# Kernel optimization log

Hardware: AMD Instinct MI355X
Metric: run time of the kernel (lower is better)

## Reference

```python
import jax, jax.numpy as jnp
import numpy as np

B, T, D = 8, 4096, 256
INNER, S = D * 2, 16          # expand=2, d_state=16
CODEBOOK, THRESH = 240, 0.7


def setup_inputs() -> dict:
    key = jax.random.key(0)
    ks = iter(jax.random.split(key, 32))
    nrm = lambda shape, s=0.02: jax.random.normal(next(ks), shape, dtype=jnp.float32) * s
    return {
        'x': jax.random.normal(next(ks), (B, T, D), dtype=jnp.float32),
        # Mamba backend params
        'in_proj_w': nrm((D, 2 * INNER)), 'in_proj_b': jnp.zeros((2 * INNER,), jnp.float32),
        'conv_proj_w': nrm((INNER, INNER)), 'conv_proj_b': jnp.zeros((INNER,), jnp.float32),
        'A_log': jax.random.normal(next(ks), (INNER, S), dtype=jnp.float32) * 0.01,
        'bc_proj_w': nrm((INNER, 2 * S)), 'bc_proj_b': jnp.zeros((2 * S,), jnp.float32),
        'dt_proj_w': nrm((INNER, INNER)), 'dt_proj_b': jnp.zeros((INNER,), jnp.float32),
        'out_proj_w': nrm((INNER, D)), 'out_proj_b': jnp.zeros((D,), jnp.float32),
        # CatastropheDetector params
        'cat1_w': nrm((D, 64)), 'cat1_b': jnp.zeros((64,), jnp.float32),
        'cat2_w': nrm((64, 32)), 'cat2_b': jnp.zeros((32,), jnp.float32),
        'risk_w': nrm((32, 1)), 'risk_b': jnp.zeros((1,), jnp.float32),
        # E8 quantizer params
        'e8a_w': nrm((D, 64)), 'e8a_b': jnp.zeros((64,), jnp.float32),
        'e8b_w': nrm((64, 8)), 'e8b_b': jnp.zeros((8,), jnp.float32),
        'e8_codebook': jax.random.normal(next(ks), (CODEBOOK, 8), dtype=jnp.float32) * 0.1,
    }


def reference(x, in_proj_w, in_proj_b, conv_proj_w, conv_proj_b, A_log,
              bc_proj_w, bc_proj_b, dt_proj_w, dt_proj_b, out_proj_w, out_proj_b,
              cat1_w, cat1_b, cat2_w, cat2_b, risk_w, risk_b,
              e8a_w, e8a_b, e8b_w, e8b_b, e8_codebook):
    # ---- Mamba selective-scan dynamics ----
    xp = x @ in_proj_w + in_proj_b                       # [B,T,2*inner]
    x_main, x_gate = jnp.split(xp, 2, axis=-1)
    x_conv = jax.nn.silu(x_main @ conv_proj_w + conv_proj_b)  # [B,T,inner]
    A = -jnp.exp(A_log)                                  # [inner,S]
    bc = x_conv @ bc_proj_w + bc_proj_b                  # [B,T,2S]
    Bp, Cp = jnp.split(bc, 2, axis=-1)                   # [B,T,S] each
    dt = jax.nn.softplus(x_conv @ dt_proj_w + dt_proj_b) # [B,T,inner]

    def step(h, ins):  # h: [B,inner,S]
        x_t, dt_t, B_t, C_t = ins                        # [B,inner],[B,inner],[B,S],[B,S]
        A_bar = jnp.exp(dt_t[..., None] * A)
        h = A_bar * h + (dt_t[..., None] * B_t[:, None, :]) * x_t[..., None]
        y_t = (h * C_t[:, None, :]).sum(-1)              # [B,inner]
        return h, y_t

    h0 = jnp.zeros((x.shape[0], A_log.shape[0], A_log.shape[1]), x.dtype)
    xs = (x_conv.transpose(1, 0, 2), dt.transpose(1, 0, 2),
          Bp.transpose(1, 0, 2), Cp.transpose(1, 0, 2))
    _, y = jax.lax.scan(step, h0, xs)                    # [T,B,inner]
    y = y.transpose(1, 0, 2) * jax.nn.silu(x_gate)
    y = y @ out_proj_w + out_proj_b                      # [B,T,D]

    # ---- Catastrophe / bifurcation detector ----
    f = jax.nn.gelu(y @ cat1_w + cat1_b)
    f = f @ cat2_w + cat2_b
    risk = jax.nn.sigmoid((f @ risk_w + risk_b).squeeze(-1))  # [B,T]
    vel = jnp.diff(y, axis=1, prepend=y[:, :1])
    vn = jnp.linalg.norm(vel, axis=-1)                   # [B,T]
    acc = jnp.abs(jnp.diff(vn, axis=1, prepend=vn[:, :1]))
    combined = 0.5 * risk + 0.3 * jax.nn.sigmoid(vn) + 0.2 * jax.nn.sigmoid(acc)
    is_bif = combined > THRESH

    # ---- E8 quantization with straight-through estimator ----
    e8c = jax.nn.gelu(y @ e8a_w + e8a_b) @ e8b_w + e8b_b # [B,T,8]
    flat = e8c.reshape(-1, 8)
    d2 = ((flat ** 2).sum(1, keepdims=True)
          - 2.0 * flat @ e8_codebook.T
          + (e8_codebook ** 2).sum(1)[None, :])          # [B*T,240]
    idx = jnp.argmin(d2, axis=1)
    q = e8_codebook[idx].reshape(e8c.shape)
    e8_codes = e8c + jax.lax.stop_gradient(q - e8c)
    return (y, e8_codes, idx.reshape(y.shape[0], y.shape[1]), is_bif)
```

## Files before the change

kernel.cpp:

```cpp
#include <hip/hip_runtime.h>
#include <hip/hip_bf16.h>
#include <math.h>

#define BB 8
#define TT 4096
#define DD 256
#define INNER 512
#define SS 16
#define MTOK (BB*TT)
#define NCODE 240

#define SCAN_NC 64
#define SCAN_L  64

typedef unsigned short u16;
typedef unsigned int   u32;
typedef __attribute__((ext_vector_type(8))) short short8;
typedef __attribute__((ext_vector_type(4))) float f32x4;

__device__ __forceinline__ float sigmoidf_(float x) { return 1.f / (1.f + expf(-x)); }
__device__ __forceinline__ float siluf_(float x)    { return x / (1.f + expf(-x)); }
__device__ __forceinline__ float geluf_(float x) {
    float x3 = x * x * x;
    return 0.5f * x * (1.f + tanhf(0.7978845608028654f * (x + 0.044715f * x3)));
}
__device__ __forceinline__ float softplusf_(float x) {
    return fmaxf(x, 0.f) + log1pf(expf(-fabsf(x)));
}

__device__ __forceinline__ u16 f2bf(float v) {
    u32 u = __float_as_uint(v);
    u32 r = (u + 0x7FFFu + ((u >> 16) & 1u)) >> 16;
    return (u16)r;
}
__device__ __forceinline__ float bf2f(u16 h) {
    return __uint_as_float(((u32)h) << 16);
}

__device__ __forceinline__ void gload16(const void* g, void* l) {
    __builtin_amdgcn_global_load_lds((const __attribute__((address_space(1))) u32*)g,
                                     (__attribute__((address_space(3))) u32*)l, 16, 0, 0);
}

template<int MODE>
__global__ __launch_bounds__(256)
void gemmS(const u16* __restrict__ Ah, const u16* __restrict__ Al, int K,
           const u16* __restrict__ BTh, const u16* __restrict__ BTl,
           const float* __restrict__ bias, int Nstore,
           float* __restrict__ out0, u16* __restrict__ oh, u16* __restrict__ ol)
{
    __shared__ u16 sm[4][128 * 32];

    const int tid  = threadIdx.x;
    const int lane = tid & 63;
    const int wv   = tid >> 6;
    const int wr   = wv >> 1;
    const int wc   = wv & 1;
    const int lc   = lane & 15;
    const int kc   = lane >> 4;
    const int row0 = blockIdx.y * 128;
    const int col0 = blockIdx.x * 128;

    const u16* Agh = Ah + (size_t)row0 * K;
    const u16* Agl = Al + (size_t)row0 * K;
    const u16* Bgh = BTh + (size_t)col0 * K;
    const u16* Bgl = BTl + (size_t)col0 * K;

    f32x4 acc[4][4];
    #pragma unroll
    for (int m = 0; m < 4; ++m)
        #pragma unroll
        for (int n = 0; n < 4; ++n) acc[m][n] = (f32x4)0.f;

    for (int k0 = 0; k0 < K; k0 += 32) {
        #pragma unroll
        for (int c = 0; c < 2; ++c) {
            int e = c * 256 + tid;
            int row = e >> 2, ch = e & 3;
            int chs = ch ^ ((row >> 1) & 3);
            size_t go = (size_t)row * K + k0 + chs * 8;
            gload16(Agh + go, &sm[0][e * 8]);
            gload16(Agl + go, &sm[1][e * 8]);
            gload16(Bgh + go, &sm[2][e * 8]);
            gload16(Bgl + go, &sm[3][e * 8]);
        }
        __syncthreads();

        short8 ah[4], al[4], bh[4], bl[4];
        #pragma unroll
        for (int m = 0; m < 4; ++m) {
            int row = wr * 64 + m * 16 + lc;
            int off = row * 32 + ((kc ^ ((row >> 1) & 3)) << 3);
            ah[m] = *(const short8*)&sm[0][off];
            al[m] = *(const short8*)&sm[1][off];
        }
        #pragma unroll
        for (int n = 0; n < 4; ++n) {
            int row = wc * 64 + n * 16 + lc;
            int off = row * 32 + ((kc ^ ((row >> 1) & 3)) << 3);
            bh[n] = *(const short8*)&sm[2][off];
            bl[n] = *(const short8*)&sm[3][off];
        }
        #pragma unroll
        for (int m = 0; m < 4; ++m)
            #pragma unroll
            for (int n = 0; n < 4; ++n) {
                acc[m][n] = __builtin_amdgcn_mfma_f32_16x16x32_bf16(ah[m], bh[n], acc[m][n], 0, 0, 0);
                acc[m][n] = __builtin_amdgcn_mfma_f32_16x16x32_bf16(ah[m], bl[n], acc[m][n], 0, 0, 0);
                acc[m][n] = __builtin_amdgcn_mfma_f32_16x16x32_bf16(al[m], bh[n], acc[m][n], 0, 0, 0);
            }
        __syncthreads();
    }

    #pragma unroll
    for (int n = 0; n < 4; ++n) {
        int colg = col0 + wc * 64 + n * 16 + lc;
        float bv = (MODE == 3) ? ((colg < Nstore) ? bias[colg] : 0.f) : bias[colg];
        #pragma unroll
        for (int m = 0; m < 4; ++m) {
            f32x4 a = acc[m][n];
            #pragma unroll
            for (int r = 0; r < 4; ++r) {
                int rowg = row0 + wr * 64 + m * 16 + kc * 4 + r;
                float v = a[r] + bv;
                if (MODE == 0) {
                    if (colg < 512) {
                        u16 hh = f2bf(v);
                        oh[(size_t)rowg * 512 + colg] = hh;
                        ol[(size_t)rowg * 512 + colg] = f2bf(v - bf2f(hh));
                    } else {
                        out0[(size_t)rowg * 512 + colg - 512] = v;
                    }
                } else if (MODE == 1) {
                    v = siluf_(v);
                    u16 hh = f2bf(v);
                    oh[(size_t)rowg * 512 + colg] = hh;
                    ol[(size_t)rowg * 512 + colg] = f2bf(v - bf2f(hh));
                } else if (MODE == 2) {
                    out0[(size_t)rowg * 512 + colg] = softplusf_(v);
                } else if (MODE == 3) {
                    if (colg < Nstore) out0[(size_t)rowg * 32 + colg] = v;
                } else if (MODE == 4) {
                    out0[(size_t)rowg * 256 + colg] = v;
                    u16 hh = f2bf(v);
                    oh[(size_t)rowg * 256 + colg] = hh;
                    ol[(size_t)rowg * 256 + colg] = f2bf(v - bf2f(hh));
                } else {
                    out0[(size_t)rowg * 128 + colg] = geluf_(v);
                }
            }
        }
    }
}

__global__ __launch_bounds__(256)
void split_kernel(const float* __restrict__ s, u16* __restrict__ h,
                  u16* __restrict__ l, int n)
{
    int i = blockIdx.x * 256 + threadIdx.x;
    if (i >= n) return;
    float v = s[i];
    u16 hh = f2bf(v);
    h[i] = hh;
    l[i] = f2bf(v - bf2f(hh));
}

__global__ __launch_bounds__(256)
void splitT_kernel(const float* __restrict__ w, u16* __restrict__ hT,
                   u16* __restrict__ lT, int K, int N, int Npad)
{
    int idx = blockIdx.x * 256 + threadIdx.x;
    if (idx >= Npad * K) return;
    int n = idx / K, k = idx - n * K;
    float v = (n < N) ? w[(size_t)k * N + n] : 0.f;
    u16 hh = f2bf(v);
    hT[idx] = hh;
    lT[idx] = f2bf(v - bf2f(hh));
}

__global__ __launch_bounds__(256)
void headprep_kernel(const float* __restrict__ c1w, const float* __restrict__ c1b,
                     const float* __restrict__ e8aw, const float* __restrict__ e8ab,
                     u16* __restrict__ hT, u16* __restrict__ lT, float* __restrict__ hb)
{
    int idx = blockIdx.x * 256 + threadIdx.x;
    if (idx < 128) hb[idx] = (idx < 64) ? c1b[idx] : e8ab[idx - 64];
    if (idx >= 128 * 256) return;
    int n = idx >> 8, k = idx & 255;
    float v = (n < 64) ? c1w[(size_t)k * 64 + n] : e8aw[(size_t)k * 64 + (n - 64)];
    u16 hh = f2bf(v);
    hT[idx] = hh;
    lT[idx] = f2bf(v - bf2f(hh));
}

__global__ __launch_bounds__(256)
void scan_pass1(const float* __restrict__ DT, const u16* __restrict__ XCh,
                const u16* __restrict__ XCl, const float* __restrict__ BC,
                const float* __restrict__ A_log,
                float* __restrict__ Pbuf, float* __restrict__ Hbuf)
{
    const int bid  = blockIdx.x;
    const int half = bid & 1;
    const int c    = (bid >> 1) & (SCAN_NC - 1);
    const int b    = bid >> 7;
    const int ch   = half * 256 + threadIdx.x;
    const int row0 = b * TT + c * SCAN_L;

    float A[16];
    {
        const float4* ar = (const float4*)(A_log + ch * 16);
        #pragma unroll
        for (int q = 0; q < 4; ++q) {
            float4 v = ar[q];
            A[q * 4 + 0] = -__expf(v.x);
            A[q * 4 + 1] = -__expf(v.y);
            A[q * 4 + 2] = -__expf(v.z);
            A[q * 4 + 3] = -__expf(v.w);
        }
    }

    float h[16];
    #pragma unroll
    for (int s = 0; s < 16; ++s) h[s] = 0.f;
    float dtsum = 0.f;

    const float* dtp = DT  + (size_t)row0 * 512 + ch;
    const u16*   xhp = XCh + (size_t)row0 * 512 + ch;
    const u16*   xlp = XCl + (size_t)row0 * 512 + ch;
    const float* bcp = BC  + (size_t)row0 * 32;

    float dv = dtp[0];
    float xv = bf2f(xhp[0]) + bf2f(xlp[0]);
    for (int t = 0; t < SCAN_L; ++t) {
        const int tn = (t + 1 < SCAN_L) ? t + 1 : t;
        float dvn = dtp[(size_t)tn * 512];
        float xvn = bf2f(xhp[(size_t)tn * 512]) + bf2f(xlp[(size_t)tn * 512]);
        const float* br = bcp + (size_t)t * 32;
        float dtx = dv * xv;
        dtsum += dv;
        #pragma unroll
        for (int s = 0; s < 16; ++s) {
            float a = __expf(dv * A[s]);
            h[s] = fmaf(a, h[s], dtx * br[s]);
        }
        dv = dvn; xv = xvn;
    }

    size_t o = ((size_t)(b * SCAN_NC + c) * 512 + ch) * 16;
    #pragma unroll
    for (int s = 0; s < 16; ++s) {
        Pbuf[o + s] = __expf(dtsum * A[s]);
        Hbuf[o + s] = h[s];
    }
}

__global__ __launch_bounds__(256)
void scan_pass2(const float* __restrict__ Pbuf, float* __restrict__ Hbuf)
{
    const int idx = blockIdx.x * 256 + threadIdx.x;
    const int b = idx >> 13;
    const int ds = idx & 8191;
    float hin = 0.f;
    for (int c = 0; c < SCAN_NC; ++c) {
        size_t o = ((size_t)(b * SCAN_NC + c)) * (INNER * SS) + ds;
        float p = Pbuf[o], hh = Hbuf[o];
        Hbuf[o] = hin;
        hin = fmaf(p, hin, hh);
    }
}

__global__ __launch_bounds__(256)
void scan_pass3(const float* __restrict__ DT, const u16* __restrict__ XCh,
                const u16* __restrict__ XCl, const float* __restrict__ BC,
                const float* __restrict__ A_log, const float* __restrict__ GATE,
                const float* __restrict__ Hin,
                u16* __restrict__ YGh, u16* __restrict__ YGl)
{
    const int bid  = blockIdx.x;
    const int half = bid & 1;
    const int c    = (bid >> 1) & (SCAN_NC - 1);
    const int b    = bid >> 7;
    const int ch   = half * 256 + threadIdx.x;
    const int row0 = b * TT + c * SCAN_L;

    float A[16];
    {
        const float4* ar = (const float4*)(A_log + ch * 16);
        #pragma unroll
        for (int q = 0; q < 4; ++q) {
            float4 v = ar[q];
            A[q * 4 + 0] = -__expf(v.x);
            A[q * 4 + 1] = -__expf(v.y);
            A[q * 4 + 2] = -__expf(v.z);
            A[q * 4 + 3] = -__expf(v.w);
        }
    }

    float h[16];
    {
        size_t o = ((size_t)(b * SCAN_NC + c) * 512 + ch) * 16;
        const float4* hr = (const float4*)(Hin + o);
        #pragma unroll
        for (int q = 0; q < 4; ++q) {
            float4 v = hr[q];
            h[q * 4 + 0] = v.x; h[q * 4 + 1] = v.y;
            h[q * 4 + 2] = v.z; h[q * 4 + 3] = v.w;
        }
    }

    const float* dtp = DT   + (size_t)row0 * 512 + ch;
    const u16*   xhp = XCh  + (size_t)row0 * 512 + ch;
    const u16*   xlp = XCl  + (size_t)row0 * 512 + ch;
    const float* gtp = GATE + (size_t)row0 * 512 + ch;
    const float* bcp = BC   + (size_t)row0 * 32;
    u16* yhp = YGh + (size_t)row0 * 512 + ch;
    u16* ylp = YGl + (size_t)row0 * 512 + ch;

    float dv = dtp[0];
    float xv = bf2f(xhp[0]) + bf2f(xlp[0]);
    float gv = gtp[0];
    for (int t = 0; t < SCAN_L; ++t) {
        const int tn = (t + 1 < SCAN_L) ? t + 1 : t;
        float dvn = dtp[(size_t)tn * 512];
        float xvn = bf2f(xhp[(size_t)tn * 512]) + bf2f(xlp[(size_t)tn * 512]);
        float gvn = gtp[(size_t)tn * 512];
        const float* br = bcp + (size_t)t * 32;
        float dtx = dv * xv;
        float y = 0.f;
        #pragma unroll
        for (int s = 0; s < 16; ++s) {
            float a = __expf(dv * A[s]);
            h[s] = fmaf(a, h[s], dtx * br[s]);
            y = fmaf(h[s], br[16 + s], y);
        }
        float yg = y * siluf_(gv);
        u16 hh = f2bf(yg);
        yhp[(size_t)t * 512] = hh;
        ylp[(size_t)t * 512] = f2bf(yg - bf2f(hh));
        dv = dvn; xv = xvn; gv = gvn;
    }
}

__global__ __launch_bounds__(256)
void head_finish(const float* __restrict__ F1,
                 const float* __restrict__ w2, const float* __restrict__ b2,
                 const float* __restrict__ w3, const float* __restrict__ b3,
                 const float* __restrict__ wb, const float* __restrict__ bb,
                 const float* __restrict__ cb,
                 float* __restrict__ risk, float* __restrict__ codes_out,
                 float* __restrict__ idx_out)
{
    __shared__ float F1s[64][129];
    __shared__ float w2S[64 * 32];
    __shared__ float wbS[64 * 8];
    __shared__ float cbS[NCODE * 8];
    __shared__ float cnS[NCODE];
    __shared__ float w3S[32];
    __shared__ float b2S[32];
    __shared__ float bbS[8];
    const int tid = threadIdx.x;
    const int tok0 = blockIdx.x * 64;

    for (int e = tid; e < 64 * 128; e += 256)
        F1s[e >> 7][e & 127] = F1[(size_t)tok0 * 128 + e];
    for (int e = tid; e < 64 * 32; e += 256) w2S[e] = w2[e];
    for (int e = tid; e < 64 * 8; e += 256) wbS[e] = wb[e];
    for (int e = tid; e < NCODE * 8; e += 256) cbS[e] = cb[e];
    if (tid < 32) { w3S[tid] = w3[tid]; b2S[tid] = b2[tid]; }
    if (tid < 8) bbS[tid] = bb[tid];
    __syncthreads();
    for (int e = tid; e < NCODE; e += 256) {
        float s = 0.f;
        #pragma unroll
        for (int q = 0; q < 8; ++q) s = fmaf(cbS[e * 8 + q], cbS[e * 8 + q], s);
        cnS[e] = s;
    }
    __syncthreads();

    const int lane = tid & 63;
    const int wv   = tid >> 6;
    const int tl   = wv * 16 + (lane >> 2);
    const int role = lane & 3;
    const float* f1c = &F1s[tl][0];
    const float* f1e = &F1s[tl][64];

    float v = 0.f;
    float bd = 3.4e38f;
    int bi = 0;

    if (role < 2) {
        float f2[16];
        #pragma unroll
        for (int d = 0; d < 16; ++d) f2[d] = b2S[role * 16 + d];
        for (int k = 0; k < 64; ++k) {
            float fv = f1c[k];
            #pragma unroll
            for (int d = 0; d < 16; ++d)
                f2[d] = fmaf(fv, w2S[k * 32 + role * 16 + d], f2[d]);
        }
        #pragma unroll
        for (int d = 0; d < 16; ++d) v = fmaf(f2[d], w3S[role * 16 + d], v);
    } else {
        float ec[8];
        #pragma unroll
        for (int q = 0; q < 8; ++q) ec[q] = bbS[q];
        for (int k = 0; k < 64; ++k) {
            float fv = f1e[k];
            #pragma unroll
            for (int q = 0; q < 8; ++q) ec[q] = fmaf(fv, wbS[k * 8 + q], ec[q]);
        }
        float fn = 0.f;
        #pragma unroll
        for (int q = 0; q < 8; ++q) fn = fmaf(ec[q], ec[q], fn);
        const int base = (role - 2) * 120;
        for (int i = 0; i < 120; ++i) {
            int cc = base + i;
            float dot = 0.f;
            #pragma unroll
            for (int q = 0; q < 8; ++q) dot = fmaf(ec[q], cbS[cc * 8 + q], dot);
            float d = fn + cnS[cc] - 2.f * dot;
            if (d < bd) { bd = d; bi = cc; }
        }
    }

    float vp = __shfl_xor(v, 1, 64);
    float od = __shfl_xor(bd, 1, 64);
    int   oi = __shfl_xor(bi, 1, 64);
    const int tok = tok0 + tl;
    if (role == 0) risk[tok] = sigmoidf_(v + vp + b3[0]);
    if (role == 2) {
        if (od < bd || (od == bd && oi < bi)) { bd = od; bi = oi; }
        idx_out[tok] = (float)bi;
        #pragma unroll
        for (int q = 0; q < 8; ++q)
            codes_out[(size_t)tok * 8 + q] = cbS[bi * 8 + q];
    }
}

__global__ __launch_bounds__(256)
void vn_kernel(const float* __restrict__ y, float* __restrict__ vn)
{
    const int tid = threadIdx.x;
    const int w = tid >> 6, j = tid & 63;
    const int t = blockIdx.x * 4 + w;
    const int tt = t & (TT - 1);
    const float4* cur = (const float4*)(y + (size_t)t * 256);
    const float4* prv = (const float4*)(y + (size_t)(tt == 0 ? t : t - 1) * 256);
    float4 a = cur[j], b = prv[j];
    float dx = a.x - b.x, dy = a.y - b.y, dz = a.z - b.z, dw = a.w - b.w;
    float ss = dx * dx + dy * dy + dz * dz + dw * dw;
    ss += __shfl_xor(ss, 1, 64);
    ss += __shfl_xor(ss, 2, 64);
    ss += __shfl_xor(ss, 4, 64);
    ss += __shfl_xor(ss, 8, 64);
    ss += __shfl_xor(ss, 16, 64);
    ss += __shfl_xor(ss, 32, 64);
    if (j == 0) vn[t] = sqrtf(ss);
}

__global__ __launch_bounds__(256)
void combined_kernel(const float* __restrict__ risk, const float* __restrict__ vn,
                     float* __restrict__ bif)
{
    const int t = blockIdx.x * 256 + threadIdx.x;
    const int tt = t & (TT - 1);
    float v = vn[t];
    float a = (tt == 0) ? 0.f : fabsf(v - vn[t - 1]);
    float cmb = 0.5f * risk[t] + 0.3f * sigmoidf_(v) + 0.2f * sigmoidf_(a);
    bif[t] = (cmb > 0.7f) ? 1.f : 0.f;
}

extern "C" void kernel_launch(void* const* d_in, const int* in_sizes, int n_in,
                              void* d_out, int out_size, void* d_ws, size_t ws_size,
                              hipStream_t stream)
{
    const float* x          = (const float*)d_in[0];
    const float* in_proj_w  = (const float*)d_in[1];
    const float* in_proj_b  = (const float*)d_in[2];
    const float* conv_w     = (const float*)d_in[3];
    const float* conv_b     = (const float*)d_in[4];
    const float* A_log      = (const float*)d_in[5];
    const float* bc_w       = (const float*)d_in[6];
    const float* bc_b       = (const float*)d_in[7];
    const float* dt_w       = (const float*)d_in[8];
    const float* dt_b       = (const float*)d_in[9];
    const float* out_w      = (const float*)d_in[10];
    const float* out_b      = (const float*)d_in[11];
    const float* cat1_w     = (const float*)d_in[12];
    const float* cat1_b     = (const float*)d_in[13];
    const float* cat2_w     = (const float*)d_in[14];
    const float* cat2_b     = (const float*)d_in[15];
    const float* risk_w     = (const float*)d_in[16];
    const float* risk_b     = (const float*)d_in[17];
    const float* e8a_w      = (const float*)d_in[18];
    const float* e8a_b      = (const float*)d_in[19];
    const float* e8b_w      = (const float*)d_in[20];
    const float* e8b_b      = (const float*)d_in[21];
    const float* codebook   = (const float*)d_in[22];

    float* out = (float*)d_out;
    float* y_out     = out;
    float* codes_out = out + (size_t)MTOK * 256;
    float* idx_out   = codes_out + (size_t)MTOK * 8;
    float* bif_out   = idx_out + MTOK;

    const size_t AL = 255;
    #define ALN(x) (((x) + AL) & ~AL)
    size_t fixed_b = 2 * ALN((size_t)MTOK * 4)
                   + 2 * ALN((size_t)MTOK * 256 * 2)
                   + 2 * ALN((size_t)MTOK * 256 * 2)
                   + ALN((size_t)MTOK * 128 * 4)
                   + 2 * ALN((size_t)1024 * 256 * 2)
                   + 2 * ALN((size_t)512 * 512 * 2)
                   + 2 * ALN((size_t)512 * 512 * 2)
                   + 2 * ALN((size_t)128 * 512 * 2)
                   + 2 * ALN((size_t)256 * 512 * 2)
                   + 2 * ALN((size_t)128 * 256 * 2)
                   + ALN((size_t)128 * 4);
    int G = 8;
    {
        const int cand[4] = {1, 2, 4, 8};
        for (int i = 0; i < 4; ++i) {
            int g = cand[i];
            size_t Mg = (size_t)MTOK / g, Bg = BB / g;
            size_t grp = 2 * ALN(Mg * 512 * 2)
                       + ALN(Mg * 512 * 4)
                       + 2 * ALN(Mg * 512 * 2)
                       + ALN(Mg * 512 * 4)
                       + ALN(Mg * 32 * 4)
                       + 2 * ALN(Bg * SCAN_NC * INNER * SS * 4);
            if (fixed_b + grp <= ws_size) { G = g; break; }
        }
    }
    const size_t Mg = (size_t)MTOK / G;
    const int    Bg = BB / G;

    char* p = (char*)d_ws;
    #define TAKE(T, name, bytes) T* name = (T*)p; p += ALN((size_t)(bytes));
    TAKE(float, risk, MTOK * 4)
    TAKE(float, vn,   MTOK * 4)
    TAKE(u16, xh, (size_t)MTOK * 256 * 2)
    TAKE(u16, xl, (size_t)MTOK * 256 * 2)
    TAKE(u16, yh, (size_t)MTOK * 256 * 2)
    TAKE(u16, yl, (size_t)MTOK * 256 * 2)
    TAKE(float, F1buf, (size_t)MTOK * 128 * 4)
    TAKE(u16, wiTh, (size_t)1024 * 256 * 2)
    TAKE(u16, wiTl, (size_t)1024 * 256 * 2)
    TAKE(u16, wcTh, (size_t)512 * 512 * 2)
    TAKE(u16, wcTl, (size_t)512 * 512 * 2)
    TAKE(u16, wdTh, (size_t)512 * 512 * 2)
    TAKE(u16, wdTl, (size_t)512 * 512 * 2)
    TAKE(u16, wbTh, (size_t)128 * 512 * 2)
    TAKE(u16, wbTl, (size_t)128 * 512 * 2)
    TAKE(u16, woTh, (size_t)256 * 512 * 2)
    TAKE(u16, woTl, (size_t)256 * 512 * 2)
    TAKE(u16, whTh, (size_t)128 * 256 * 2)
    TAKE(u16, whTl, (size_t)128 * 256 * 2)
    TAKE(float, hbias, 128 * 4)
    TAKE(u16, MAINh, Mg * 512 * 2)
    TAKE(u16, MAINl, Mg * 512 * 2)
    TAKE(float, GATE, Mg * 512 * 4)
    TAKE(u16, XCh, Mg * 512 * 2)
    TAKE(u16, XCl, Mg * 512 * 2)
    TAKE(float, DT, Mg * 512 * 4)
    TAKE(float, BC, Mg * 32 * 4)
    TAKE(float, Pb, (size_t)Bg * SCAN_NC * INNER * SS * 4)
    TAKE(float, Hb, (size_t)Bg * SCAN_NC * INNER * SS * 4)

    split_kernel<<<(MTOK * 256 + 255) / 256, 256, 0, stream>>>(x, xh, xl, MTOK * 256);
    splitT_kernel<<<(1024 * 256 + 255) / 256, 256, 0, stream>>>(in_proj_w, wiTh, wiTl, 256, 1024, 1024);
    splitT_kernel<<<(512 * 512 + 255) / 256, 256, 0, stream>>>(conv_w, wcTh, wcTl, 512, 512, 512);
    splitT_kernel<<<(512 * 512 + 255) / 256, 256, 0, stream>>>(dt_w, wdTh, wdTl, 512, 512, 512);
    splitT_kernel<<<(128 * 512 + 255) / 256, 256, 0, stream>>>(bc_w, wbTh, wbTl, 512, 32, 128);
    splitT_kernel<<<(256 * 512 + 255) / 256, 256, 0, stream>>>(out_w, woTh, woTl, 512, 256, 256);
    headprep_kernel<<<128, 256, 0, stream>>>(cat1_w, cat1_b, e8a_w, e8a_b, whTh, whTl, hbias);

    for (int g = 0; g < G; ++g) {
        const u16* xgh = xh + (size_t)g * Mg * 256;
        const u16* xgl = xl + (size_t)g * Mg * 256;
        float* yg_out  = y_out + (size_t)g * Mg * 256;
        u16* ygh = yh + (size_t)g * Mg * 256;
        u16* ygl = yl + (size_t)g * Mg * 256;

        gemmS<0><<<dim3(8, Mg / 128), 256, 0, stream>>>(
            xgh, xgl, 256, wiTh, wiTl, in_proj_b, 1024, GATE, MAINh, MAINl);
        gemmS<1><<<dim3(4, Mg / 128), 256, 0, stream>>>(
            MAINh, MAINl, 512, wcTh, wcTl, conv_b, 512, nullptr, XCh, XCl);
        gemmS<2><<<dim3(4, Mg / 128), 256, 0, stream>>>(
            XCh, XCl, 512, wdTh, wdTl, dt_b, 512, DT, nullptr, nullptr);
        gemmS<3><<<dim3(1, Mg / 128), 256, 0, stream>>>(
            XCh, XCl, 512, wbTh, wbTl, bc_b, 32, BC, nullptr, nullptr);
        scan_pass1<<<Bg * SCAN_NC * 2, 256, 0, stream>>>(DT, XCh, XCl, BC, A_log, Pb, Hb);
        scan_pass2<<<Bg * 32, 256, 0, stream>>>(Pb, Hb);
        scan_pass3<<<Bg * SCAN_NC * 2, 256, 0, stream>>>(DT, XCh, XCl, BC, A_log, GATE,
                                                         Hb, MAINh, MAINl);
        gemmS<4><<<dim3(2, Mg / 128), 256, 0, stream>>>(
            MAINh, MAINl, 512, woTh, woTl, out_b, 256, yg_out, ygh, ygl);
    }

    gemmS<5><<<dim3(1, MTOK / 128), 256, 0, stream>>>(
        yh, yl, 256, whTh, whTl, hbias, 128, F1buf, nullptr, nullptr);
    head_finish<<<MTOK / 64, 256, 0, stream>>>(F1buf, cat2_w, cat2_b, risk_w, risk_b,
                                               e8b_w, e8b_b, codebook,
                                               risk, codes_out, idx_out);
    vn_kernel<<<MTOK / 4, 256, 0, stream>>>(y_out, vn);
    combined_kernel<<<MTOK / 256, 256, 0, stream>>>(risk, vn, bif_out);
}
```

Baseline: 843.0 us.

## Run full batch in one pass with aliased workspace, fuse dt/bc GEMMs and weight prep

Removes the group loop that split the batch when workspace was short. It now runs every stage once over all tokens and aliases buffers (DT over MAIN, XC over x, F1 over GATE, scan partials in the y output region) so the workspace fits. The dt and bc projections are merged into one GEMM with a 640-wide padded weight, and all weight-transpose and split prep kernels become a single launch. In-place aliasing adds risk: scan_pass3 writes into the XC buffer it reads, and scan scratch shares the y output region, so correctness depends on read/write ordering.

```diff
diff --git a/kernel.cpp b/kernel.cpp
--- a/kernel.cpp
+++ b/kernel.cpp
@@ -46,8 +46,9 @@
 __global__ __launch_bounds__(256)
 void gemmS(const u16* __restrict__ Ah, const u16* __restrict__ Al, int K,
            const u16* __restrict__ BTh, const u16* __restrict__ BTl,
-           const float* __restrict__ bias, int Nstore,
-           float* __restrict__ out0, u16* __restrict__ oh, u16* __restrict__ ol)
+           const float* __restrict__ bias,
+           float* __restrict__ out0, float* __restrict__ out1,
+           u16* __restrict__ oh, u16* __restrict__ ol)
 {
     __shared__ u16 sm[4][128 * 32];
 
@@ -115,7 +116,7 @@
     #pragma unroll
     for (int n = 0; n < 4; ++n) {
         int colg = col0 + wc * 64 + n * 16 + lc;
-        float bv = (MODE == 3) ? ((colg < Nstore) ? bias[colg] : 0.f) : bias[colg];
+        float bv = bias[colg];
         #pragma unroll
         for (int m = 0; m < 4; ++m) {
             f32x4 a = acc[m][n];
@@ -137,9 +138,11 @@
                     oh[(size_t)rowg * 512 + colg] = hh;
                     ol[(size_t)rowg * 512 + colg] = f2bf(v - bf2f(hh));
                 } else if (MODE == 2) {
-                    out0[(size_t)rowg * 512 + colg] = softplusf_(v);
-                } else if (MODE == 3) {
-                    if (colg < Nstore) out0[(size_t)rowg * 32 + colg] = v;
+                    if (colg < 512) {
+                        out0[(size_t)rowg * 512 + colg] = softplusf_(v);
+                    } else if (colg < 544) {
+                        out1[(size_t)rowg * 32 + colg - 512] = v;
+                    }
                 } else if (MODE == 4) {
                     out0[(size_t)rowg * 256 + colg] = v;
                     u16 hh = f2bf(v);
@@ -166,31 +169,49 @@
 }
 
 __global__ __launch_bounds__(256)
-void splitT_kernel(const float* __restrict__ w, u16* __restrict__ hT,
-                   u16* __restrict__ lT, int K, int N, int Npad)
+void prep_weights(const float* __restrict__ in_proj_w, const float* __restrict__ conv_w,
+                  const float* __restrict__ dt_w, const float* __restrict__ bc_w,
+                  const float* __restrict__ out_w,
+                  const float* __restrict__ cat1_w, const float* __restrict__ e8a_w,
+                  const float* __restrict__ dt_b, const float* __restrict__ bc_b,
+                  const float* __restrict__ cat1_b, const float* __restrict__ e8a_b,
+                  u16* __restrict__ wiTh, u16* __restrict__ wiTl,
+                  u16* __restrict__ wcTh, u16* __restrict__ wcTl,
+                  u16* __restrict__ wdbTh, u16* __restrict__ wdbTl,
+                  u16* __restrict__ woTh, u16* __restrict__ woTl,
+                  u16* __restrict__ whTh, u16* __restrict__ whTl,
+                  float* __restrict__ dbbias, float* __restrict__ hbias)
 {
     int idx = blockIdx.x * 256 + threadIdx.x;
-    if (idx >= Npad * K) return;
-    int n = idx / K, k = idx - n * K;
-    float v = (n < N) ? w[(size_t)k * N + n] : 0.f;
-    u16 hh = f2bf(v);
-    hT[idx] = hh;
-    lT[idx] = f2bf(v - bf2f(hh));
-}
-
-__global__ __launch_bounds__(256)
-void headprep_kernel(const float* __restrict__ c1w, const float* __restrict__ c1b,
-                     const float* __restrict__ e8aw, const float* __restrict__ e8ab,
-                     u16* __restrict__ hT, u16* __restrict__ lT, float* __restrict__ hb)
-{
-    int idx = blockIdx.x * 256 + threadIdx.x;
-    if (idx < 128) hb[idx] = (idx < 64) ? c1b[idx] : e8ab[idx - 64];
-    if (idx >= 128 * 256) return;
-    int n = idx >> 8, k = idx & 255;
-    float v = (n < 64) ? c1w[(size_t)k * 64 + n] : e8aw[(size_t)k * 64 + (n - 64)];
-    u16 hh = f2bf(v);
-    hT[idx] = hh;
-    lT[idx] = f2bf(v - bf2f(hh));
+    float v; u16 *dh, *dl; int off;
+    if (idx < 262144) {
+        int e = idx, n = e >> 8, k = e & 255;
+        v = in_proj_w[(size_t)k * 1024 + n]; dh = wiTh; dl = wiTl; off = e;
+    } else if (idx < 524288) {
+        int e = idx - 262144, n = e >> 9, k = e & 511;
+        v = conv_w[(size_t)k * 512 + n]; dh = wcTh; dl = wcTl; off = e;
+    } else if (idx < 851968) {
+        int e = idx - 524288, n = e >> 9, k = e & 511;
+        v = (n < 512) ? dt_w[(size_t)k * 512 + n]
+                      : ((n < 544) ? bc_w[(size_t)k * 32 + (n - 512)] : 0.f);
+        dh = wdbTh; dl = wdbTl; off = e;
+    } else if (idx < 983040) {
+        int e = idx - 851968, n = e >> 9, k = e & 511;
+        v = out_w[(size_t)k * 256 + n]; dh = woTh; dl = woTl; off = e;
+    } else if (idx < 1015808) {
+        int e = idx - 983040, n = e >> 8, k = e & 255;
+        v = (n < 64) ? cat1_w[(size_t)k * 64 + n] : e8a_w[(size_t)k * 64 + (n - 64)];
+        dh = whTh; dl = whTl; off = e;
+    } else if (idx < 1015808 + 640) {
+        int i = idx - 1015808;
+        dbbias[i] = (i < 512) ? dt_b[i] : ((i < 544) ? bc_b[i - 512] : 0.f);
+        return;
+    } else if (idx < 1015808 + 640 + 128) {
+        int i = idx - 1015808 - 640;
+        hbias[i] = (i < 64) ? cat1_b[i] : e8a_b[i - 64];
+        return;
+    } else return;
+    u16 hh = f2bf(v); dh[off] = hh; dl[off] = f2bf(v - bf2f(hh));
 }
 
 __global__ __launch_bounds__(256)
@@ -506,101 +527,62 @@
 
     const size_t AL = 255;
     #define ALN(x) (((x) + AL) & ~AL)
-    size_t fixed_b = 2 * ALN((size_t)MTOK * 4)
-                   + 2 * ALN((size_t)MTOK * 256 * 2)
-                   + 2 * ALN((size_t)MTOK * 256 * 2)
-                   + ALN((size_t)MTOK * 128 * 4)
-                   + 2 * ALN((size_t)1024 * 256 * 2)
-                   + 2 * ALN((size_t)512 * 512 * 2)
-                   + 2 * ALN((size_t)512 * 512 * 2)
-                   + 2 * ALN((size_t)128 * 512 * 2)
-                   + 2 * ALN((size_t)256 * 512 * 2)
-                   + 2 * ALN((size_t)128 * 256 * 2)
-                   + ALN((size_t)128 * 4);
-    int G = 8;
-    {
-        const int cand[4] = {1, 2, 4, 8};
-        for (int i = 0; i < 4; ++i) {
-            int g = cand[i];
-            size_t Mg = (size_t)MTOK / g, Bg = BB / g;
-            size_t grp = 2 * ALN(Mg * 512 * 2)
-                       + ALN(Mg * 512 * 4)
-                       + 2 * ALN(Mg * 512 * 2)
-                       + ALN(Mg * 512 * 4)
-                       + ALN(Mg * 32 * 4)
-                       + 2 * ALN(Bg * SCAN_NC * INNER * SS * 4);
-            if (fixed_b + grp <= ws_size) { G = g; break; }
-        }
-    }
-    const size_t Mg = (size_t)MTOK / G;
-    const int    Bg = BB / G;
-
     char* p = (char*)d_ws;
     #define TAKE(T, name, bytes) T* name = (T*)p; p += ALN((size_t)(bytes));
     TAKE(float, risk, MTOK * 4)
     TAKE(float, vn,   MTOK * 4)
-    TAKE(u16, xh, (size_t)MTOK * 256 * 2)
-    TAKE(u16, xl, (size_t)MTOK * 256 * 2)
-    TAKE(u16, yh, (size_t)MTOK * 256 * 2)
-    TAKE(u16, yl, (size_t)MTOK * 256 * 2)
-    TAKE(float, F1buf, (size_t)MTOK * 128 * 4)
     TAKE(u16, wiTh, (size_t)1024 * 256 * 2)
     TAKE(u16, wiTl, (size_t)1024 * 256 * 2)
     TAKE(u16, wcTh, (size_t)512 * 512 * 2)
     TAKE(u16, wcTl, (size_t)512 * 512 * 2)
-    TAKE(u16, wdTh, (size_t)512 * 512 * 2)
-    TAKE(u16, wdTl, (size_t)512 * 512 * 2)
-    TAKE(u16, wbTh, (size_t)128 * 512 * 2)
-    TAKE(u16, wbTl, (size_t)128 * 512 * 2)
+    TAKE(u16, wdbTh, (size_t)640 * 512 * 2)
+    TAKE(u16, wdbTl, (size_t)640 * 512 * 2)
     TAKE(u16, woTh, (size_t)256 * 512 * 2)
     TAKE(u16, woTl, (size_t)256 * 512 * 2)
     TAKE(u16, whTh, (size_t)128 * 256 * 2)
     TAKE(u16, whTl, (size_t)128 * 256 * 2)
+    TAKE(float, dbbias, 640 * 4)
     TAKE(float, hbias, 128 * 4)
-    TAKE(u16, MAINh, Mg * 512 * 2)
-    TAKE(u16, MAINl, Mg * 512 * 2)
-    TAKE(float, GATE, Mg * 512 * 4)
-    TAKE(u16, XCh, Mg * 512 * 2)
-    TAKE(u16, XCl, Mg * 512 * 2)
-    TAKE(float, DT, Mg * 512 * 4)
-    TAKE(float, BC, Mg * 32 * 4)
-    TAKE(float, Pb, (size_t)Bg * SCAN_NC * INNER * SS * 4)
-    TAKE(float, Hb, (size_t)Bg * SCAN_NC * INNER * SS * 4)
+    TAKE(u16, A0, (size_t)2 * MTOK * 512 * 2)
+    TAKE(u16, B0, (size_t)2 * MTOK * 512 * 2)
+    TAKE(float, GATE, (size_t)MTOK * 512 * 4)
+    TAKE(float, BC, (size_t)MTOK * 32 * 4)
+
+    u16* MAINh = A0;
+    u16* MAINl = A0 + (size_t)MTOK * 512;
+    float* DT  = (float*)A0;
+    u16* yh    = A0;
+    u16* yl    = A0 + (size_t)MTOK * 512;
+    u16* xh  = B0;
+    u16* xl  = B0 + (size_t)MTOK * 512;
+    u16* XCh = B0;
+    u16* XCl = B0 + (size_t)MTOK * 512;
+    float* F1 = GATE;
+    float* Pb = y_out;
+    float* Hb = y_out + (size_t)MTOK * 128;
 
     split_kernel<<<(MTOK * 256 + 255) / 256, 256, 0, stream>>>(x, xh, xl, MTOK * 256);
-    splitT_kernel<<<(1024 * 256 + 255) / 256, 256, 0, stream>>>(in_proj_w, wiTh, wiTl, 256, 1024, 1024);
-    splitT_kernel<<<(512 * 512 + 255) / 256, 256, 0, stream>>>(conv_w, wcTh, wcTl, 512, 512, 512);
-    splitT_kernel<<<(512 * 512 + 255) / 256, 256, 0, stream>>>(dt_w, wdTh, wdTl, 512, 512, 512);
-    splitT_kernel<<<(128 * 512 + 255) / 256, 256, 0, stream>>>(bc_w, wbTh, wbTl, 512, 32, 128);
-    splitT_kernel<<<(256 * 512 + 255) / 256, 256, 0, stream>>>(out_w, woTh, woTl, 512, 256, 256);
-    headprep_kernel<<<128, 256, 0, stream>>>(cat1_w, cat1_b, e8a_w, e8a_b, whTh, whTl, hbias);
-
-    for (int g = 0; g < G; ++g) {
-        const u16* xgh = xh + (size_t)g * Mg * 256;
-        const u16* xgl = xl + (size_t)g * Mg * 256;
-        float* yg_out  = y_out + (size_t)g * Mg * 256;
-        u16* ygh = yh + (size_t)g * Mg * 256;
-        u16* ygl = yl + (size_t)g * Mg * 256;
-
-        gemmS<0><<<dim3(8, Mg / 128), 256, 0, stream>>>(
-            xgh, xgl, 256, wiTh, wiTl, in_proj_b, 1024, GATE, MAINh, MAINl);
-        gemmS<1><<<dim3(4, Mg / 128), 256, 0, stream>>>(
-            MAINh, MAINl, 512, wcTh, wcTl, conv_b, 512, nullptr, XCh, XCl);
-        gemmS<2><<<dim3(4, Mg / 128), 256, 0, stream>>>(
-            XCh, XCl, 512, wdTh, wdTl, dt_b, 512, DT, nullptr, nullptr);
-        gemmS<3><<<dim3(1, Mg / 128), 256, 0, stream>>>(
-            XCh, XCl, 512, wbTh, wbTl, bc_b, 32, BC, nullptr, nullptr);
-        scan_pass1<<<Bg * SCAN_NC * 2, 256, 0, stream>>>(DT, XCh, XCl, BC, A_log, Pb, Hb);
-        scan_pass2<<<Bg * 32, 256, 0, stream>>>(Pb, Hb);
-        scan_pass3<<<Bg * SCAN_NC * 2, 256, 0, stream>>>(DT, XCh, XCl, BC, A_log, GATE,
-                                                         Hb, MAINh, MAINl);
-        gemmS<4><<<dim3(2, Mg / 128), 256, 0, stream>>>(
-            MAINh, MAINl, 512, woTh, woTl, out_b, 256, yg_out, ygh, ygl);
-    }
-
+    prep_weights<<<(1016576 + 255) / 256, 256, 0, stream>>>(
+        in_proj_w, conv_w, dt_w, bc_w, out_w, cat1_w, e8a_w,
+        dt_b, bc_b, cat1_b, e8a_b,
+        wiTh, wiTl, wcTh, wcTl, wdbTh, wdbTl, woTh, woTl, whTh, whTl,
+        dbbias, hbias);
+
+    gemmS<0><<<dim3(8, MTOK / 128), 256, 0, stream>>>(
+        xh, xl, 256, wiTh, wiTl, in_proj_b, GATE, nullptr, MAINh, MAINl);
+    gemmS<1><<<dim3(4, MTOK / 128), 256, 0, stream>>>(
+        MAINh, MAINl, 512, wcTh, wcTl, conv_b, nullptr, nullptr, XCh, XCl);
+    gemmS<2><<<dim3(5, MTOK / 128), 256, 0, stream>>>(
+        XCh, XCl, 512, wdbTh, wdbTl, dbbias, DT, BC, nullptr, nullptr);
+    scan_pass1<<<BB * SCAN_NC * 2, 256, 0, stream>>>(DT, XCh, XCl, BC, A_log, Pb, Hb);
+    scan_pass2<<<256, 256, 0, stream>>>(Pb, Hb);
+    scan_pass3<<<BB * SCAN_NC * 2, 256, 0, stream>>>(DT, XCh, XCl, BC, A_log, GATE,
+                                                     Hb, XCh, XCl);
+    gemmS<4><<<dim3(2, MTOK / 128), 256, 0, stream>>>(
+        XCh, XCl, 512, woTh, woTl, out_b, y_out, nullptr, yh, yl);
     gemmS<5><<<dim3(1, MTOK / 128), 256, 0, stream>>>(
-        yh, yl, 256, whTh, whTl, hbias, 128, F1buf, nullptr, nullptr);
-    head_finish<<<MTOK / 64, 256, 0, stream>>>(F1buf, cat2_w, cat2_b, risk_w, risk_b,
+        yh, yl, 256, whTh, whTl, hbias, F1, nullptr, nullptr, nullptr);
+    head_finish<<<MTOK / 64, 256, 0, stream>>>(F1, cat2_w, cat2_b, risk_w, risk_b,
                                                e8b_w, e8b_b, codebook,
                                                risk, codes_out, idx_out);
     vn_kernel<<<MTOK / 4, 256, 0, stream>>>(y_out, vn);
```

After: 956.0 us. +13.4%, slower.
